# Kernel tuning notes

Hardware: AMD Instinct MI355X
Metric: run time of the kernel (lower is better)

## Reference

```python
import jax, jax.numpy as jnp
import numpy as np

# NSA hyperparameters (HFNSACore defaults)
KS, ST, BS = 32, 16, 64            # kernel_size, stride, block_size
TOP_N, NINIT, NLOCAL, WIN = 16, 2, 1, 512
NEG = -1e30
BIG = 1e30


def setup_inputs() -> dict:
    key = jax.random.key(0)
    k1, k2, k3, k4 = jax.random.split(key, 4)
    T, Hq, Hkv, D = 2048, 16, 1, 128
    q = jax.random.normal(k1, (T, Hq, D), jnp.float32)
    k = jax.random.normal(k2, (T, Hkv, D), jnp.float32)
    v = jax.random.normal(k3, (T, Hkv, D), jnp.float32)
    combine_weight = jax.random.normal(k4, (T, Hq, 3), jnp.float32)
    cu_seqlens = jnp.array([0, T], dtype=jnp.int32)  # single varlen sequence
    return {"q": q, "k": k, "v": v, "combine_weight": combine_weight, "cu_seqlens": cu_seqlens}


def _nsa_forward(q, k, v, cw):
    T, Hq, Dqk = q.shape
    Hkv = k.shape[1]
    G = Hq // Hkv                      # GQA group size
    Dv = v.shape[-1]
    scale = Dqk ** -0.5
    M = (T - KS) // ST + 1             # number of compressed kv tokens
    NB = (T + BS - 1) // BS            # number of selection blocks
    t_pos = jnp.arange(T)

    # ---- CompressKV (version='mean'): mean-pool sliding blocks of size KS, stride ST ----
    blk_idx = jnp.arange(M)[:, None] * ST + jnp.arange(KS)[None, :]   # [M, KS]
    cmp_k = k[blk_idx].mean(axis=1)    # [M, Hkv, Dqk]
    cmp_v = v[blk_idx].mean(axis=1)    # [M, Hkv, Dv]

    qg = q.reshape(T, Hkv, G, Dqk)

    # ---- compress_attn: causal attention over compressed kv ----
    # query t can see cmp token j only if its block is fully in the past: j*ST + KS <= t+1
    cmp_scores = jnp.einsum('tkgd,mkd->tkgm', qg, cmp_k) * scale      # [T,Hkv,G,M]
    cmp_valid = (jnp.arange(M)[None, :] * ST + KS) <= (t_pos[:, None] + 1)  # [T,M]
    cmp_scores = jnp.where(cmp_valid[:, None, None, :], cmp_scores, NEG)
    p_cmp = jax.nn.softmax(cmp_scores, axis=-1)
    p_cmp = jnp.where(cmp_valid.any(-1)[:, None, None, None], p_cmp, 0.0)
    cmp_o = jnp.einsum('tkgm,mkd->tkgd', p_cmp, cmp_v).reshape(T, Hq, Dv)

    # ---- slc_topk_indices: map cmp probs to selection-block scores (scale_slc_p) ----
    ju, bu = KS // ST, BS // ST        # extents in stride units
    j = np.arange(M)[:, None]
    b = np.arange(NB)[None, :]
    ov = np.maximum(0, np.minimum(j + ju, (b + 1) * bu) - np.maximum(j, b * bu))
    Wmap = jnp.asarray(ov / ju, jnp.float32)                          # [M, NB] overlap fraction
    slc_p = jnp.einsum('tkgm,mb->tkb', p_cmp, Wmap)                   # sum probs over group heads
    cur_blk = t_pos // BS
    bidx = jnp.arange(NB)
    future = bidx[None, :] > cur_blk[:, None]                         # [T,NB]
    forced = (bidx[None, :] < NINIT) | ((bidx[None, :] <= cur_blk[:, None]) & (bidx[None, :] > cur_blk[:, None] - NLOCAL))
    slc_p = jnp.where(future[:, None, :], NEG, slc_p)
    slc_p = jnp.where(forced[:, None, :], BIG, slc_p)
    topk = jax.lax.top_k(slc_p, TOP_N)[1]                             # [T,Hkv,TOP_N]

    causal = t_pos[:, None] >= t_pos[None, :]                         # [T,T]

    # ---- select_attn: causal attention restricted to selected blocks ----
    key_blk = t_pos // BS
    sel = (topk[..., None] == key_blk[None, None, None, :]).any(axis=2)  # [T,Hkv,T]
    smask = sel & causal[:, None, :]
    slc_scores = jnp.einsum('tkgd,skd->tkgs', qg, k) * scale
    slc_scores = jnp.where(smask[:, :, None, :], slc_scores, NEG)
    slc_o = jnp.einsum('tkgs,skd->tkgd', jax.nn.softmax(slc_scores, axis=-1), v).reshape(T, Hq, Dv)

    # ---- swa_varlen_func: sliding-window causal attention ----
    wmask = causal & ((t_pos[:, None] - t_pos[None, :]) < WIN)
    swa_scores = jnp.einsum('tkgd,skd->tkgs', qg, k) * scale
    swa_scores = jnp.where(wmask[None, None, :, :].transpose(2, 0, 1, 3)[:, :, 0:1, :].squeeze(2)[:, None, None, :] if False else wmask[:, None, None, :], swa_scores, NEG)
    swa_o = jnp.einsum('tkgs,skd->tkgd', jax.nn.softmax(swa_scores, axis=-1), v).reshape(T, Hq, Dv)

    # ---- fused_sigmoid_combine ----
    w = jax.nn.sigmoid(cw)                                            # [T,Hq,3]
    return w[..., 0:1] * cmp_o + w[..., 1:2] * slc_o + w[..., 2:3] * swa_o


def reference(q, k, v, combine_weight, cu_seqlens):
    # single-sequence varlen: cu_seqlens = [0, T]
    return _nsa_forward(q, k, v, combine_weight)
```

## Files before the change

### kernel.cpp

```cpp
#include <hip/hip_runtime.h>
#include <math.h>

constexpr int kT    = 2048;
constexpr int kHQ   = 16;
constexpr int kD    = 128;
constexpr int kKS   = 32;
constexpr int kST   = 16;
constexpr int kBS   = 64;
constexpr int kM    = (kT - kKS) / kST + 1;
constexpr int kNB   = (kT + kBS - 1) / kBS;
constexpr int kTopN = 16;
constexpr int kNInit = 2;
constexpr int kWIN  = 512;
constexpr float kNEG = -1e30f;
constexpr float kScale = 0.08838834764831845f;
constexpr float kScaleL2 = kScale * 1.4426950408889634f;

constexpr int kPSt = 72;
constexpr int kPL  = 136;

constexpr int kPS0 = 0;
constexpr int kPS1 = 2304;
constexpr int kDmp = 4608;
constexpr int kMl  = 8704;
constexpr int kShm = 8832;

typedef __attribute__((ext_vector_type(8))) short short8;
typedef __attribute__((ext_vector_type(4))) short short4v;
typedef __attribute__((ext_vector_type(8))) _Float16 half8;
typedef __attribute__((ext_vector_type(4))) _Float16 half4v;
typedef __attribute__((ext_vector_type(4))) float floatx4;

__device__ inline short f2bf(float x) {
    unsigned u = __float_as_uint(x);
    unsigned r = (u + 0x7fffu + ((u >> 16) & 1u)) >> 16;
    return (short)r;
}
__device__ inline float b2f(short h) {
    return __uint_as_float(((unsigned)(unsigned short)h) << 16);
}

__global__ __launch_bounds__(256) void k_stage(
        const float* __restrict__ k, const float* __restrict__ v,
        short* __restrict__ kb2, _Float16* __restrict__ vt2,
        short* __restrict__ ck2h, short* __restrict__ ck2l,
        short* __restrict__ cv2) {
    const int bid = blockIdx.x;
    const int tid = threadIdx.x;
    __shared__ _Float16 vls[64 * 132];

    if (bid < 32) {
        const int b = bid;
        #pragma unroll
        for (int p = 0; p < 4; ++p) {
            const int idx = p * 256 + tid;
            const int g = idx >> 6;
            const int lane2 = idx & 63;
            const int kt = g >> 2, c = g & 3;
            const int l15v = lane2 & 15, quadv = lane2 >> 4;
            const float* src = k + (size_t)(b * 64 + kt * 16 + l15v) * kD + c * 32 + quadv * 8;
            const float4 f0 = *(const float4*)(src);
            const float4 f1 = *(const float4*)(src + 4);
            short8 s;
            s[0] = f2bf(f0.x); s[1] = f2bf(f0.y); s[2] = f2bf(f0.z); s[3] = f2bf(f0.w);
            s[4] = f2bf(f1.x); s[5] = f2bf(f1.y); s[6] = f2bf(f1.z); s[7] = f2bf(f1.w);
            *(short8*)(kb2 + ((size_t)b * 1024 + idx) * 8) = s;
        }
    } else if (bid < 64) {
        const int b = bid - 32;
        #pragma unroll
        for (int p = 0; p < 8; ++p) {
            const int idx = p * 256 + tid;
            const int r = idx >> 5;
            const int d4 = (idx & 31) * 4;
            const float4 f = *(const float4*)(v + (size_t)(b * 64 + r) * kD + d4);
            _Float16* dst = &vls[r * 132 + d4];
            dst[0] = (_Float16)f.x; dst[1] = (_Float16)f.y;
            dst[2] = (_Float16)f.z; dst[3] = (_Float16)f.w;
        }
        __syncthreads();
        #pragma unroll
        for (int p = 0; p < 4; ++p) {
            const int idx = p * 256 + tid;
            const int g = idx >> 6;
            const int lane2 = idx & 63;
            const int n8 = g >> 1, kc = g & 1;
            const int l15v = lane2 & 15, quadv = lane2 >> 4;
            half8 h;
            #pragma unroll
            for (int j = 0; j < 8; ++j) {
                const int col = kc * 32 + quadv * 8 + j;
                const int w = (col & 3) * 16 + (col >> 2);
                h[j] = vls[w * 132 + n8 * 16 + l15v];
            }
            *(half8*)(vt2 + ((size_t)b * 1024 + idx) * 8) = h;
        }
    } else {
        const int m = (bid - 64) * 2 + (tid >> 7);
        const int d = tid & 127;
        float sk = 0.f, sv = 0.f;
        if (m < kM) {
            const int base = m * kST;
            #pragma unroll
            for (int i = 0; i < kKS; ++i) {
                sk += k[(size_t)(base + i) * kD + d];
                sv += v[(size_t)(base + i) * kD + d];
            }
            sk *= (1.0f / kKS);
            sv *= (1.0f / kKS);
        }
        const short hi = f2bf(sk);
        const short lo = f2bf(sk - b2f(hi));
        const int mt = m >> 4, l15m = m & 15;
        const int c = d >> 5, quadv = (d >> 3) & 3, j = d & 7;
        const int kdst = ((mt * 4 + c) * 64 + quadv * 16 + l15m) * 8 + j;
        ck2h[kdst] = hi;
        ck2l[kdst] = lo;
        const int nt = d >> 4, l15d = d & 15;
        const int pc = (m & 64) + 4 * (m & 15) + ((m & 63) >> 4);
        const int cp = pc >> 5, quadp = (pc >> 3) & 3, jp = pc & 7;
        cv2[((nt * 4 + cp) * 64 + quadp * 16 + l15d) * 8 + jp] = f2bf(sv);
    }
}

__global__ __launch_bounds__(128, 4) void k_nsa(
        const float* __restrict__ q, const float* __restrict__ cw,
        const short* __restrict__ ck2h, const short* __restrict__ ck2l,
        const short* __restrict__ cv2, const short* __restrict__ kb2,
        const _Float16* __restrict__ vt2, float* __restrict__ out) {
    const int tid = threadIdx.x;
    const int wave = tid >> 6;
    const int lane = tid & 63;
    const int l15 = lane & 15;
    const int quad = lane >> 4;
    const int t = kT - 1 - blockIdx.x;

    __shared__ float sp[kNB];
    __shared__ unsigned selm_s;
    __shared__ __align__(16) char shm[kShm];

    _Float16* const PSme = (_Float16*)(shm + (wave ? kPS1 : kPS0));

    short8 qh[4];
    {
        const float* qp = q + ((size_t)t * kHQ + l15) * kD + quad * 8;
        #pragma unroll
        for (int c = 0; c < 4; ++c) {
            const float4 f0 = *(const float4*)(qp + c * 32);
            const float4 f1 = *(const float4*)(qp + c * 32 + 4);
            const float xs[8] = {f0.x, f0.y, f0.z, f0.w, f1.x, f1.y, f1.z, f1.w};
            #pragma unroll
            for (int j = 0; j < 8; ++j) qh[c][j] = f2bf(xs[j] * kScaleL2);
        }
    }

    const int nvalid = (t >= kKS - 1) ? min(kM, (t - (kKS - 1)) / kST + 1) : 0;
    const int cur = t >> 6;

    if (wave == 0) {
        short8 ql[4];
        {
            const float* qp = q + ((size_t)t * kHQ + l15) * kD + quad * 8;
            #pragma unroll
            for (int c = 0; c < 4; ++c) {
                const float4 f0 = *(const float4*)(qp + c * 32);
                const float4 f1 = *(const float4*)(qp + c * 32 + 4);
                const float xs[8] = {f0.x, f0.y, f0.z, f0.w, f1.x, f1.y, f1.z, f1.w};
                #pragma unroll
                for (int j = 0; j < 8; ++j)
                    ql[c][j] = f2bf(xs[j] * kScaleL2 - b2f(qh[c][j]));
            }
        }
        short* const p_lds = (short*)shm;
        floatx4 sacc[8];
        #pragma unroll
        for (int mt = 0; mt < 8; ++mt) {
            sacc[mt] = (floatx4){0, 0, 0, 0};
            #pragma unroll
            for (int c = 0; c < 4; ++c) {
                const short8 Ah = *(const short8*)(ck2h + ((mt * 4 + c) * 64 + lane) * 8);
                const short8 Al = *(const short8*)(ck2l + ((mt * 4 + c) * 64 + lane) * 8);
                sacc[mt] = __builtin_amdgcn_mfma_f32_16x16x32_bf16(Ah, qh[c], sacc[mt], 0, 0, 0);
                sacc[mt] = __builtin_amdgcn_mfma_f32_16x16x32_bf16(Ah, ql[c], sacc[mt], 0, 0, 0);
                sacc[mt] = __builtin_amdgcn_mfma_f32_16x16x32_bf16(Al, qh[c], sacc[mt], 0, 0, 0);
            }
        }
        float mx = kNEG;
        #pragma unroll
        for (int mt = 0; mt < 8; ++mt)
            #pragma unroll
            for (int r = 0; r < 4; ++r) {
                const int m = mt * 16 + quad * 4 + r;
                const float s = (m < nvalid) ? sacc[mt][r] : kNEG;
                sacc[mt][r] = s;
                mx = fmaxf(mx, s);
            }
        mx = fmaxf(mx, __shfl_xor(mx, 16));
        mx = fmaxf(mx, __shfl_xor(mx, 32));
        float sum = 0.f;
        #pragma unroll
        for (int mt = 0; mt < 8; ++mt)
            #pragma unroll
            for (int r = 0; r < 4; ++r) {
                const int m = mt * 16 + quad * 4 + r;
                const float ev = (m < nvalid) ? exp2f(sacc[mt][r] - mx) : 0.f;
                sacc[mt][r] = ev;
                sum += ev;
            }
        sum += __shfl_xor(sum, 16);
        sum += __shfl_xor(sum, 32);
        const float inv = (nvalid > 0) ? (1.f / sum) : 0.f;

        float Z[8], Y[8];
        #pragma unroll
        for (int mt = 0; mt < 8; ++mt) {
            const float p0 = sacc[mt][0] * inv, p1 = sacc[mt][1] * inv;
            const float p2 = sacc[mt][2] * inv, p3 = sacc[mt][3] * inv;
            sacc[mt][0] = p0; sacc[mt][1] = p1; sacc[mt][2] = p2; sacc[mt][3] = p3;
            Z[mt] = p0 + p1 + p2 + 0.5f * p3;
            Y[mt] = p3;
        }
        #pragma unroll
        for (int g = 0; g < 2; ++g)
            #pragma unroll
            for (int r = 0; r < 4; ++r) {
                short4v s4;
                s4[0] = f2bf(sacc[4 * g + 0][r]); s4[1] = f2bf(sacc[4 * g + 1][r]);
                s4[2] = f2bf(sacc[4 * g + 2][r]); s4[3] = f2bf(sacc[4 * g + 3][r]);
                *(short4v*)&p_lds[l15 * kPL + g * 64 + 16 * quad + 4 * r] = s4;
            }
        #pragma unroll
        for (int mt = 0; mt < 8; ++mt) {
            #pragma unroll
            for (int o = 1; o <= 8; o <<= 1) {
                Z[mt] += __shfl_xor(Z[mt], o, 16);
                Y[mt] += __shfl_xor(Y[mt], o, 16);
            }
        }
        const int srcl = ((quad + 3) & 3) * 16 + l15;
        #pragma unroll
        for (int mt = 0; mt < 8; ++mt) {
            const float up  = __shfl(Y[mt], srcl);
            const float upm = __shfl(Y[(mt + 7) & 7], srcl);
            const float pv = quad ? up : (mt ? upm : 0.f);
            const int b = 4 * mt + quad;
            float x = Z[mt] + 0.5f * pv;
            if (b > cur) x = kNEG;
            if (b < kNInit || b == cur) x = 1e30f;
            if (l15 == 0) sp[b] = x;
        }
        bool selp = false;
        if (lane < kNB) {
            const float xv = sp[lane];
            int rank = 0;
            #pragma unroll
            for (int b2 = 0; b2 < kNB; ++b2) {
                const float y = sp[b2];
                rank += (y > xv || (y == xv && b2 < lane)) ? 1 : 0;
            }
            selp = rank < kTopN;
        }
        const unsigned sm = (unsigned)__ballot(selp);
        if (lane == 0) selm_s = sm;

        short8 ap[4];
        #pragma unroll
        for (int c = 0; c < 4; ++c)
            ap[c] = *(const short8*)&p_lds[l15 * kPL + c * 32 + quad * 8];
        float w0h[4];
        #pragma unroll
        for (int r = 0; r < 4; ++r) {
            const int h = quad * 4 + r;
            const float cwa = cw[((size_t)t * kHQ + h) * 3 + 0];
            w0h[r] = 1.f / (1.f + __expf(-cwa));
        }
        #pragma unroll
        for (int nt = 0; nt < 8; ++nt) {
            floatx4 oc = (floatx4){0, 0, 0, 0};
            #pragma unroll
            for (int c = 0; c < 4; ++c) {
                const short8 bv = *(const short8*)(cv2 + ((nt * 4 + c) * 64 + lane) * 8);
                oc = __builtin_amdgcn_mfma_f32_16x16x32_bf16(ap[c], bv, oc, 0, 0, 0);
            }
            #pragma unroll
            for (int r = 0; r < 4; ++r) {
                const int h = quad * 4 + r;
                out[((size_t)t * kHQ + h) * kD + nt * 16 + l15] = w0h[r] * oc[r];
            }
        }
    }
    __syncthreads();

    const unsigned selm = selm_s;
    const int lob = max(0, (t - (kWIN - 1)) >> 6);
    const unsigned lm = 0xFFFFFFFFu >> (31 - cur);

    {
        float mS = kNEG, lS = 0.f;
        floatx4 osel[8];
        #pragma unroll
        for (int n8 = 0; n8 < 8; ++n8) osel[n8] = (floatx4){0, 0, 0, 0};

        unsigned a = selm & lm;
        int bi = 0;
        while (a) {
            const int b = __builtin_ctz(a);
            a &= a - 1u;
            const bool mine = ((bi & 1) != wave);
            ++bi;
            if (!mine) continue;

            const short* kbb = kb2 + ((size_t)b * 1024 + lane) * 8;
            floatx4 acc[4];
            {
                short8 kreg[2][4];
                #pragma unroll
                for (int kt = 0; kt < 2; ++kt)
                    #pragma unroll
                    for (int c = 0; c < 4; ++c)
                        kreg[kt][c] = *(const short8*)(kbb + (kt * 4 + c) * 512);
                #pragma unroll
                for (int kt = 0; kt < 2; ++kt) {
                    acc[kt] = (floatx4){0, 0, 0, 0};
                    #pragma unroll
                    for (int c = 0; c < 4; ++c)
                        acc[kt] = __builtin_amdgcn_mfma_f32_16x16x32_bf16(kreg[kt][c], qh[c], acc[kt], 0, 0, 0);
                }
                #pragma unroll
                for (int kt = 0; kt < 2; ++kt)
                    #pragma unroll
                    for (int c = 0; c < 4; ++c)
                        kreg[kt][c] = *(const short8*)(kbb + ((kt + 2) * 4 + c) * 512);
                #pragma unroll
                for (int kt = 0; kt < 2; ++kt) {
                    acc[kt + 2] = (floatx4){0, 0, 0, 0};
                    #pragma unroll
                    for (int c = 0; c < 4; ++c)
                        acc[kt + 2] = __builtin_amdgcn_mfma_f32_16x16x32_bf16(kreg[kt][c], qh[c], acc[kt + 2], 0, 0, 0);
                }
            }

            const int kbo = b * kBS + quad * 4;
            float bm = kNEG;
            #pragma unroll
            for (int kt = 0; kt < 4; ++kt)
                #pragma unroll
                for (int r = 0; r < 4; ++r) {
                    const int key = kbo + kt * 16 + r;
                    if (key <= t) bm = fmaxf(bm, acc[kt][r]);
                }
            bm = fmaxf(bm, __shfl_xor(bm, 16));
            bm = fmaxf(bm, __shfl_xor(bm, 32));
            const float mn = fmaxf(mS, bm);
            const float al = exp2f(mS - mn);

            float sum = 0.f;
            #pragma unroll
            for (int r = 0; r < 4; ++r) {
                half4v hs;
                #pragma unroll
                for (int kt = 0; kt < 4; ++kt) {
                    const int key = kbo + kt * 16 + r;
                    const float e0 = (key <= t) ? exp2f(acc[kt][r] - mn) : 0.f;
                    sum += e0;
                    hs[kt] = (_Float16)e0;
                }
                *(half4v*)&PSme[l15 * kPSt + 16 * quad + 4 * r] = hs;
            }
            sum += __shfl_xor(sum, 16);
            sum += __shfl_xor(sum, 32);
            lS = lS * al + sum; mS = mn;

            float alh[4];
            #pragma unroll
            for (int r = 0; r < 4; ++r) alh[r] = __shfl(al, quad * 4 + r);
            const half8 ap0 = *(const half8*)&PSme[l15 * kPSt + quad * 8];
            const half8 ap1 = *(const half8*)&PSme[l15 * kPSt + 32 + quad * 8];
            const _Float16* vtb = vt2 + ((size_t)b * 1024 + lane) * 8;
            {
                half8 vr[4][2];
                #pragma unroll
                for (int n8 = 0; n8 < 4; ++n8) {
                    vr[n8][0] = *(const half8*)(vtb + (n8 * 2 + 0) * 512);
                    vr[n8][1] = *(const half8*)(vtb + (n8 * 2 + 1) * 512);
                }
                #pragma unroll
                for (int n8 = 0; n8 < 4; ++n8) {
                    #pragma unroll
                    for (int r = 0; r < 4; ++r) osel[n8][r] *= alh[r];
                    osel[n8] = __builtin_amdgcn_mfma_f32_16x16x32_f16(ap0, vr[n8][0], osel[n8], 0, 0, 0);
                    osel[n8] = __builtin_amdgcn_mfma_f32_16x16x32_f16(ap1, vr[n8][1], osel[n8], 0, 0, 0);
                }
                #pragma unroll
                for (int n8 = 0; n8 < 4; ++n8) {
                    vr[n8][0] = *(const half8*)(vtb + ((n8 + 4) * 2 + 0) * 512);
                    vr[n8][1] = *(const half8*)(vtb + ((n8 + 4) * 2 + 1) * 512);
                }
                #pragma unroll
                for (int n8 = 0; n8 < 4; ++n8) {
                    #pragma unroll
                    for (int r = 0; r < 4; ++r) osel[n8 + 4][r] *= alh[r];
                    osel[n8 + 4] = __builtin_amdgcn_mfma_f32_16x16x32_f16(ap0, vr[n8][0], osel[n8 + 4], 0, 0, 0);
                    osel[n8 + 4] = __builtin_amdgcn_mfma_f32_16x16x32_f16(ap1, vr[n8][1], osel[n8 + 4], 0, 0, 0);
                }
            }
        }

        if (wave == 1) {
            short* const dmp = (short*)(shm + kDmp);
            #pragma unroll
            for (int n8 = 0; n8 < 8; ++n8) {
                short4v s4;
                #pragma unroll
                for (int r = 0; r < 4; ++r) s4[r] = f2bf(osel[n8][r]);
                *(short4v*)&dmp[lane * 32 + n8 * 4] = s4;
            }
            if (quad == 0) ((float2*)(shm + kMl))[l15] = make_float2(mS, lS);
        }
        __syncthreads();
        if (wave == 0) {
            const short* const ox1 = (const short*)(shm + kDmp);
            const float2* const ml1 = (const float2*)(shm + kMl);
            #pragma unroll
            for (int r = 0; r < 4; ++r) {
                const int h = quad * 4 + r;
                const float m0 = __shfl(mS, h), l0 = __shfl(lS, h);
                const float2 s1 = ml1[h];
                const float mM = fmaxf(m0, s1.x);
                const float c0 = exp2f(m0 - mM);
                const float c1 = exp2f(s1.x - mM);
                const float li = 1.f / (l0 * c0 + s1.y * c1);
                const float cwb = cw[((size_t)t * kHQ + h) * 3 + 1];
                const float w1 = 1.f / (1.f + __expf(-cwb));
                float* op = out + ((size_t)t * kHQ + h) * kD + l15;
                #pragma unroll
                for (int n8 = 0; n8 < 8; ++n8) {
                    const float sM = (osel[n8][r] * c0 + b2f(ox1[lane * 32 + n8 * 4 + r]) * c1) * li;
                    op[n8 * 16] += w1 * sM;
                }
            }
        }
    }

    float mW = kNEG, lW = 0.f;
    floatx4 oswa[8];
    #pragma unroll
    for (int n8 = 0; n8 < 8; ++n8) oswa[n8] = (floatx4){0, 0, 0, 0};
    {
        unsigned a = lm & ~((1u << lob) - 1u);
        int bi = 0;
        while (a) {
            const int b = __builtin_ctz(a);
            a &= a - 1u;
            const bool mine = ((bi & 1) != wave);
            ++bi;
            if (!mine) continue;

            const short* kbb = kb2 + ((size_t)b * 1024 + lane) * 8;
            floatx4 acc[4];
            {
                short8 kreg[2][4];
                #pragma unroll
                for (int kt = 0; kt < 2; ++kt)
                    #pragma unroll
                    for (int c = 0; c < 4; ++c)
                        kreg[kt][c] = *(const short8*)(kbb + (kt * 4 + c) * 512);
                #pragma unroll
                for (int kt = 0; kt < 2; ++kt) {
                    acc[kt] = (floatx4){0, 0, 0, 0};
                    #pragma unroll
                    for (int c = 0; c < 4; ++c)
                        acc[kt] = __builtin_amdgcn_mfma_f32_16x16x32_bf16(kreg[kt][c], qh[c], acc[kt], 0, 0, 0);
                }
                #pragma unroll
                for (int kt = 0; kt < 2; ++kt)
                    #pragma unroll
                    for (int c = 0; c < 4; ++c)
                        kreg[kt][c] = *(const short8*)(kbb + ((kt + 2) * 4 + c) * 512);
                #pragma unroll
                for (int kt = 0; kt < 2; ++kt) {
                    acc[kt + 2] = (floatx4){0, 0, 0, 0};
                    #pragma unroll
                    for (int c = 0; c < 4; ++c)
                        acc[kt + 2] = __builtin_amdgcn_mfma_f32_16x16x32_bf16(kreg[kt][c], qh[c], acc[kt + 2], 0, 0, 0);
                }
            }

            const int kbo = b * kBS + quad * 4;
            float bm = kNEG;
            #pragma unroll
            for (int kt = 0; kt < 4; ++kt)
                #pragma unroll
                for (int r = 0; r < 4; ++r) {
                    const int key = kbo + kt * 16 + r;
                    if (key <= t && (t - key) < kWIN) bm = fmaxf(bm, acc[kt][r]);
                }
            bm = fmaxf(bm, __shfl_xor(bm, 16));
            bm = fmaxf(bm, __shfl_xor(bm, 32));
            const float mn = fmaxf(mW, bm);
            const float al = exp2f(mW - mn);

            float sum = 0.f;
            #pragma unroll
            for (int r = 0; r < 4; ++r) {
                half4v hw;
                #pragma unroll
                for (int kt = 0; kt < 4; ++kt) {
                    const int key = kbo + kt * 16 + r;
                    const float e0 = (key <= t && (t - key) < kWIN) ? exp2f(acc[kt][r] - mn) : 0.f;
                    sum += e0;
                    hw[kt] = (_Float16)e0;
                }
                *(half4v*)&PSme[l15 * kPSt + 16 * quad + 4 * r] = hw;
            }
            sum += __shfl_xor(sum, 16);
            sum += __shfl_xor(sum, 32);
            lW = lW * al + sum; mW = mn;

            float alh[4];
            #pragma unroll
            for (int r = 0; r < 4; ++r) alh[r] = __shfl(al, quad * 4 + r);
            const half8 ap0 = *(const half8*)&PSme[l15 * kPSt + quad * 8];
            const half8 ap1 = *(const half8*)&PSme[l15 * kPSt + 32 + quad * 8];
            const _Float16* vtb = vt2 + ((size_t)b * 1024 + lane) * 8;
            {
                half8 vr[4][2];
                #pragma unroll
                for (int n8 = 0; n8 < 4; ++n8) {
                    vr[n8][0] = *(const half8*)(vtb + (n8 * 2 + 0) * 512);
                    vr[n8][1] = *(const half8*)(vtb + (n8 * 2 + 1) * 512);
                }
                #pragma unroll
                for (int n8 = 0; n8 < 4; ++n8) {
                    #pragma unroll
                    for (int r = 0; r < 4; ++r) oswa[n8][r] *= alh[r];
                    oswa[n8] = __builtin_amdgcn_mfma_f32_16x16x32_f16(ap0, vr[n8][0], oswa[n8], 0, 0, 0);
                    oswa[n8] = __builtin_amdgcn_mfma_f32_16x16x32_f16(ap1, vr[n8][1], oswa[n8], 0, 0, 0);
                }
                #pragma unroll
                for (int n8 = 0; n8 < 4; ++n8) {
                    vr[n8][0] = *(const half8*)(vtb + ((n8 + 4) * 2 + 0) * 512);
                    vr[n8][1] = *(const half8*)(vtb + ((n8 + 4) * 2 + 1) * 512);
                }
                #pragma unroll
                for (int n8 = 0; n8 < 4; ++n8) {
                    #pragma unroll
                    for (int r = 0; r < 4; ++r) oswa[n8 + 4][r] *= alh[r];
                    oswa[n8 + 4] = __builtin_amdgcn_mfma_f32_16x16x32_f16(ap0, vr[n8][0], oswa[n8 + 4], 0, 0, 0);
                    oswa[n8 + 4] = __builtin_amdgcn_mfma_f32_16x16x32_f16(ap1, vr[n8][1], oswa[n8 + 4], 0, 0, 0);
                }
            }
        }
    }

    __syncthreads();
    if (wave == 1) {
        short* const dmp = (short*)(shm + kDmp);
        #pragma unroll
        for (int n8 = 0; n8 < 8; ++n8) {
            short4v w4;
            #pragma unroll
            for (int r = 0; r < 4; ++r) w4[r] = f2bf(oswa[n8][r]);
            *(short4v*)&dmp[lane * 32 + n8 * 4] = w4;
        }
        if (quad == 0) ((float2*)(shm + kMl))[l15] = make_float2(mW, lW);
    }
    __syncthreads();
    if (wave == 0) {
        const short* const ox1 = (const short*)(shm + kDmp);
        const float2* const ml1 = (const float2*)(shm + kMl);
        #pragma unroll
        for (int r = 0; r < 4; ++r) {
            const int h = quad * 4 + r;
            const float m0 = __shfl(mW, h), l0 = __shfl(lW, h);
            const float2 s1 = ml1[h];
            const float mM = fmaxf(m0, s1.x);
            const float c0 = exp2f(m0 - mM);
            const float c1 = exp2f(s1.x - mM);
            const float li = 1.f / (l0 * c0 + s1.y * c1);
            const float cwc = cw[((size_t)t * kHQ + h) * 3 + 2];
            const float w2 = 1.f / (1.f + __expf(-cwc));
            float* op = out + ((size_t)t * kHQ + h) * kD + l15;
            #pragma unroll
            for (int n8 = 0; n8 < 8; ++n8) {
                const float wM = (oswa[n8][r] * c0 + b2f(ox1[lane * 32 + n8 * 4 + r]) * c1) * li;
                op[n8 * 16] += w2 * wM;
            }
        }
    }
}

extern "C" void kernel_launch(void* const* d_in, const int* in_sizes, int n_in,
                              void* d_out, int out_size, void* d_ws, size_t ws_size,
                              hipStream_t stream) {
    const float* q  = (const float*)d_in[0];
    const float* k  = (const float*)d_in[1];
    const float* v  = (const float*)d_in[2];
    const float* cw = (const float*)d_in[3];
    float* out = (float*)d_out;

    short* kb2    = (short*)d_ws;
    _Float16* vt2 = (_Float16*)(kb2 + 32 * 1024 * 8);
    short* ck2h   = (short*)(vt2 + 32 * 1024 * 8);
    short* ck2l   = ck2h + 32 * 64 * 8;
    short* cv2    = ck2l + 32 * 64 * 8;

    k_stage<<<dim3(128), dim3(256), 0, stream>>>(k, v, kb2, vt2, ck2h, ck2l, cv2);
    k_nsa<<<dim3(kT), dim3(128), 0, stream>>>(q, cw, ck2h, ck2l, cv2, kb2, vt2, out);
}
```

Before: 158.5 us.

## Split output head dimension across two blocks per query token

Launches two blocks per query position, each computing half of the value/output dimension (4 of 8 column tiles) for the compressed, selected and sliding-window branches. This halves the accumulator registers and the V loads per block and doubles the grid, aiming for more parallelism and occupancy. The QK score computation, softmax statistics and top-k selection are now duplicated in both blocks, doubling that work and the Q/K traffic. The shared-memory dump stride shrinks to match the smaller accumulator.

```diff
diff --git a/kernel.cpp b/kernel.cpp
--- a/kernel.cpp
+++ b/kernel.cpp
@@ -22,8 +22,9 @@
 constexpr int kPS0 = 0;
 constexpr int kPS1 = 2304;
 constexpr int kDmp = 4608;
-constexpr int kMl  = 8704;
-constexpr int kShm = 8832;
+constexpr int kDS  = 20;
+constexpr int kMl  = 7168;
+constexpr int kShm = 7296;
 
 typedef __attribute__((ext_vector_type(8))) short short8;
 typedef __attribute__((ext_vector_type(4))) short short4v;
@@ -133,7 +134,8 @@
     const int lane = tid & 63;
     const int l15 = lane & 15;
     const int quad = lane >> 4;
-    const int t = kT - 1 - blockIdx.x;
+    const int hf = blockIdx.x & 1;
+    const int t = kT - 1 - (blockIdx.x >> 1);
 
     __shared__ float sp[kNB];
     __shared__ unsigned selm_s;
@@ -275,7 +277,8 @@
             w0h[r] = 1.f / (1.f + __expf(-cwa));
         }
         #pragma unroll
-        for (int nt = 0; nt < 8; ++nt) {
+        for (int nt2 = 0; nt2 < 4; ++nt2) {
+            const int nt = hf * 4 + nt2;
             floatx4 oc = (floatx4){0, 0, 0, 0};
             #pragma unroll
             for (int c = 0; c < 4; ++c) {
@@ -297,9 +300,9 @@
 
     {
         float mS = kNEG, lS = 0.f;
-        floatx4 osel[8];
-        #pragma unroll
-        for (int n8 = 0; n8 < 8; ++n8) osel[n8] = (floatx4){0, 0, 0, 0};
+        floatx4 osel[4];
+        #pragma unroll
+        for (int n8 = 0; n8 < 4; ++n8) osel[n8] = (floatx4){0, 0, 0, 0};
 
         unsigned a = selm & lm;
         int bi = 0;
@@ -377,43 +380,30 @@
             const half8 ap0 = *(const half8*)&PSme[l15 * kPSt + quad * 8];
             const half8 ap1 = *(const half8*)&PSme[l15 * kPSt + 32 + quad * 8];
             const _Float16* vtb = vt2 + ((size_t)b * 1024 + lane) * 8;
-            {
-                half8 vr[4][2];
-                #pragma unroll
-                for (int n8 = 0; n8 < 4; ++n8) {
-                    vr[n8][0] = *(const half8*)(vtb + (n8 * 2 + 0) * 512);
-                    vr[n8][1] = *(const half8*)(vtb + (n8 * 2 + 1) * 512);
-                }
-                #pragma unroll
-                for (int n8 = 0; n8 < 4; ++n8) {
-                    #pragma unroll
-                    for (int r = 0; r < 4; ++r) osel[n8][r] *= alh[r];
-                    osel[n8] = __builtin_amdgcn_mfma_f32_16x16x32_f16(ap0, vr[n8][0], osel[n8], 0, 0, 0);
-                    osel[n8] = __builtin_amdgcn_mfma_f32_16x16x32_f16(ap1, vr[n8][1], osel[n8], 0, 0, 0);
-                }
-                #pragma unroll
-                for (int n8 = 0; n8 < 4; ++n8) {
-                    vr[n8][0] = *(const half8*)(vtb + ((n8 + 4) * 2 + 0) * 512);
-                    vr[n8][1] = *(const half8*)(vtb + ((n8 + 4) * 2 + 1) * 512);
-                }
-                #pragma unroll
-                for (int n8 = 0; n8 < 4; ++n8) {
-                    #pragma unroll
-                    for (int r = 0; r < 4; ++r) osel[n8 + 4][r] *= alh[r];
-                    osel[n8 + 4] = __builtin_amdgcn_mfma_f32_16x16x32_f16(ap0, vr[n8][0], osel[n8 + 4], 0, 0, 0);
-                    osel[n8 + 4] = __builtin_amdgcn_mfma_f32_16x16x32_f16(ap1, vr[n8][1], osel[n8 + 4], 0, 0, 0);
-                }
+            half8 vr[4][2];
+            #pragma unroll
+            for (int n8 = 0; n8 < 4; ++n8) {
+                const int ng = hf * 4 + n8;
+                vr[n8][0] = *(const half8*)(vtb + (ng * 2 + 0) * 512);
+                vr[n8][1] = *(const half8*)(vtb + (ng * 2 + 1) * 512);
+            }
+            #pragma unroll
+            for (int n8 = 0; n8 < 4; ++n8) {
+                #pragma unroll
+                for (int r = 0; r < 4; ++r) osel[n8][r] *= alh[r];
+                osel[n8] = __builtin_amdgcn_mfma_f32_16x16x32_f16(ap0, vr[n8][0], osel[n8], 0, 0, 0);
+                osel[n8] = __builtin_amdgcn_mfma_f32_16x16x32_f16(ap1, vr[n8][1], osel[n8], 0, 0, 0);
             }
         }
 
         if (wave == 1) {
             short* const dmp = (short*)(shm + kDmp);
             #pragma unroll
-            for (int n8 = 0; n8 < 8; ++n8) {
+            for (int n8 = 0; n8 < 4; ++n8) {
                 short4v s4;
                 #pragma unroll
                 for (int r = 0; r < 4; ++r) s4[r] = f2bf(osel[n8][r]);
-                *(short4v*)&dmp[lane * 32 + n8 * 4] = s4;
+                *(short4v*)&dmp[lane * kDS + n8 * 4] = s4;
             }
             if (quad == 0) ((float2*)(shm + kMl))[l15] = make_float2(mS, lS);
         }
@@ -434,18 +424,18 @@
                 const float w1 = 1.f / (1.f + __expf(-cwb));
                 float* op = out + ((size_t)t * kHQ + h) * kD + l15;
                 #pragma unroll
-                for (int n8 = 0; n8 < 8; ++n8) {
-                    const float sM = (osel[n8][r] * c0 + b2f(ox1[lane * 32 + n8 * 4 + r]) * c1) * li;
-                    op[n8 * 16] += w1 * sM;
+                for (int n8 = 0; n8 < 4; ++n8) {
+                    const float sM = (osel[n8][r] * c0 + b2f(ox1[lane * kDS + n8 * 4 + r]) * c1) * li;
+                    op[(hf * 4 + n8) * 16] += w1 * sM;
                 }
             }
         }
     }
 
     float mW = kNEG, lW = 0.f;
-    floatx4 oswa[8];
+    floatx4 oswa[4];
     #pragma unroll
-    for (int n8 = 0; n8 < 8; ++n8) oswa[n8] = (floatx4){0, 0, 0, 0};
+    for (int n8 = 0; n8 < 4; ++n8) oswa[n8] = (floatx4){0, 0, 0, 0};
     {
         unsigned a = lm & ~((1u << lob) - 1u);
         int bi = 0;
@@ -523,32 +513,19 @@
             const half8 ap0 = *(const half8*)&PSme[l15 * kPSt + quad * 8];
             const half8 ap1 = *(const half8*)&PSme[l15 * kPSt + 32 + quad * 8];
             const _Float16* vtb = vt2 + ((size_t)b * 1024 + lane) * 8;
-            {
-                half8 vr[4][2];
-                #pragma unroll
-                for (int n8 = 0; n8 < 4; ++n8) {
-                    vr[n8][0] = *(const half8*)(vtb + (n8 * 2 + 0) * 512);
-                    vr[n8][1] = *(const half8*)(vtb + (n8 * 2 + 1) * 512);
-                }
-                #pragma unroll
-                for (int n8 = 0; n8 < 4; ++n8) {
-                    #pragma unroll
-                    for (int r = 0; r < 4; ++r) oswa[n8][r] *= alh[r];
-                    oswa[n8] = __builtin_amdgcn_mfma_f32_16x16x32_f16(ap0, vr[n8][0], oswa[n8], 0, 0, 0);
-                    oswa[n8] = __builtin_amdgcn_mfma_f32_16x16x32_f16(ap1, vr[n8][1], oswa[n8], 0, 0, 0);
-                }
-                #pragma unroll
-                for (int n8 = 0; n8 < 4; ++n8) {
-                    vr[n8][0] = *(const half8*)(vtb + ((n8 + 4) * 2 + 0) * 512);
-                    vr[n8][1] = *(const half8*)(vtb + ((n8 + 4) * 2 + 1) * 512);
-                }
-                #pragma unroll
-                for (int n8 = 0; n8 < 4; ++n8) {
-                    #pragma unroll
-                    for (int r = 0; r < 4; ++r) oswa[n8 + 4][r] *= alh[r];
-                    oswa[n8 + 4] = __builtin_amdgcn_mfma_f32_16x16x32_f16(ap0, vr[n8][0], oswa[n8 + 4], 0, 0, 0);
-                    oswa[n8 + 4] = __builtin_amdgcn_mfma_f32_16x16x32_f16(ap1, vr[n8][1], oswa[n8 + 4], 0, 0, 0);
-                }
+            half8 vr[4][2];
+            #pragma unroll
+            for (int n8 = 0; n8 < 4; ++n8) {
+                const int ng = hf * 4 + n8;
+                vr[n8][0] = *(const half8*)(vtb + (ng * 2 + 0) * 512);
+                vr[n8][1] = *(const half8*)(vtb + (ng * 2 + 1) * 512);
+            }
+            #pragma unroll
+            for (int n8 = 0; n8 < 4; ++n8) {
+                #pragma unroll
+                for (int r = 0; r < 4; ++r) oswa[n8][r] *= alh[r];
+                oswa[n8] = __builtin_amdgcn_mfma_f32_16x16x32_f16(ap0, vr[n8][0], oswa[n8], 0, 0, 0);
+                oswa[n8] = __builtin_amdgcn_mfma_f32_16x16x32_f16(ap1, vr[n8][1], oswa[n8], 0, 0, 0);
             }
         }
     }
@@ -557,11 +534,11 @@
     if (wave == 1) {
         short* const dmp = (short*)(shm + kDmp);
         #pragma unroll
-        for (int n8 = 0; n8 < 8; ++n8) {
+        for (int n8 = 0; n8 < 4; ++n8) {
             short4v w4;
             #pragma unroll
             for (int r = 0; r < 4; ++r) w4[r] = f2bf(oswa[n8][r]);
-            *(short4v*)&dmp[lane * 32 + n8 * 4] = w4;
+            *(short4v*)&dmp[lane * kDS + n8 * 4] = w4;
         }
         if (quad == 0) ((float2*)(shm + kMl))[l15] = make_float2(mW, lW);
     }
@@ -582,9 +559,9 @@
             const float w2 = 1.f / (1.f + __expf(-cwc));
             float* op = out + ((size_t)t * kHQ + h) * kD + l15;
             #pragma unroll
-            for (int n8 = 0; n8 < 8; ++n8) {
-                const float wM = (oswa[n8][r] * c0 + b2f(ox1[lane * 32 + n8 * 4 + r]) * c1) * li;
-                op[n8 * 16] += w2 * wM;
+            for (int n8 = 0; n8 < 4; ++n8) {
+                const float wM = (oswa[n8][r] * c0 + b2f(ox1[lane * kDS + n8 * 4 + r]) * c1) * li;
+                op[(hf * 4 + n8) * 16] += w2 * wM;
             }
         }
     }
@@ -606,5 +583,5 @@
     short* cv2    = ck2l + 32 * 64 * 8;
 
     k_stage<<<dim3(128), dim3(256), 0, stream>>>(k, v, kb2, vt2, ck2h, ck2l, cv2);
-    k_nsa<<<dim3(kT), dim3(128), 0, stream>>>(q, cw, ck2h, ck2l, cv2, kb2, vt2, out);
+    k_nsa<<<dim3(2 * kT), dim3(128), 0, stream>>>(q, cw, ck2h, ck2l, cv2, kb2, vt2, out);
 }
```

Result: slower. 189.6 us (+19.6%).
